# Performance work log

Measured on AMD Instinct MI355X. Metric: run time of the kernel, lower is better.

## Reference

```python
import jax, jax.numpy as jnp
import numpy as np
import math

N_HEAD, HEAD_DIM = 12, 64
TAU = 1.0


def setup_inputs() -> dict:
    key = jax.random.key(0)
    ks = jax.random.split(key, 4)
    B, T, C = 2, 2048, 768
    x = jax.random.normal(ks[0], (B, T, C), jnp.float32)
    # Linear params (stored as [in, out]; math-equivalent to torch's x @ W.T + b).
    # 0.02 init scale keeps attention logits in a realistic range.
    w_attn = jax.random.normal(ks[1], (C, 3 * N_HEAD * HEAD_DIM), jnp.float32) * 0.02
    b_attn = jnp.zeros((3 * N_HEAD * HEAD_DIM,), jnp.float32)
    w_proj = jax.random.normal(ks[2], (N_HEAD * HEAD_DIM, C), jnp.float32) * 0.02
    b_proj = jnp.zeros((C,), jnp.float32)
    return {"x": x, "w_attn": w_attn, "b_attn": b_attn, "w_proj": w_proj, "b_proj": b_proj}


def reference(x, w_attn, b_attn, w_proj, b_proj):
    B, T, C = x.shape
    nh, hd, tau = N_HEAD, HEAD_DIM, TAU

    qkv = x @ w_attn + b_attn                              # [B,T,3*nh*hd]
    q, k, v = jnp.split(qkv, 3, axis=2)
    to_heads = lambda t: t.reshape(B, T, nh, hd).transpose(0, 2, 1, 3)  # [B,nh,T,hd]
    q, k, v = to_heads(q), to_heads(k), to_heads(v)

    att = jnp.einsum('bhqd,bhkd->bhqk', q, k) * (1.0 / math.sqrt(hd))   # [B,nh,T,T]
    causal = jnp.tril(jnp.ones((T, T), bool))
    att = jnp.where(causal, att, -jnp.inf)

    # Memory-penalty built from head 0 scores.
    S = jax.nn.relu(att[:, 0])                             # [B,T,T]; relu(-inf)=0
    col = jnp.arange(T)
    keep = (col[None, :] != 0) & (col[:, None] != col[None, :])  # zero col 0 and diagonal
    S = S * keep
    # roll rows down by 1 with row 0 zeroed
    S_shifted = jnp.concatenate([jnp.zeros((B, 1, T), S.dtype), S[:, :-1]], axis=1)
    FF = jnp.cumsum(S_shifted, axis=-2)[:, None]           # [B,1,T,T]
    FF_sum = jnp.clip(FF, 0.0, tau).sum(axis=-1)           # [B,1,T]
    positions = jnp.arange(T, dtype=x.dtype).reshape(1, 1, T, 1)
    M = positions - FF_sum / tau                           # broadcasts to [1,B,T,T] (as torch does)

    att = jax.nn.softmax(att - FF, axis=-1)
    y = jnp.einsum('bhqk,bhkd->bhqd', att, v)              # [B,nh,T,hd]
    y = y.transpose(0, 2, 1, 3).reshape(B, T, nh * hd)
    y = y @ w_proj + b_proj
    return (y, M)
```

## Files before the change

kernel.cpp:

```cpp
#include <hip/hip_runtime.h>
#include <cstddef>

#define TT 2048
#define BB 2
#define CC 768
#define NH 12
#define HD 64
#define N3 2304
#define Y_ELEMS (BB*TT*CC)
#define M_ELEMS (BB*TT*TT)

typedef __attribute__((ext_vector_type(8))) short bf16x8;
typedef __attribute__((ext_vector_type(4))) float f32x4;

__device__ inline unsigned short f2b(float f) {
  union { float f; unsigned u; } v; v.f = f;
  unsigned r = (v.u + 0x7FFFu + ((v.u >> 16) & 1u)) >> 16;
  return (unsigned short)r;
}
__device__ inline float b2f(unsigned short u) {
  union { unsigned u; float f; } v; v.u = (unsigned)u << 16; return v.f;
}

__device__ inline void gload_lds16(const unsigned short* g, unsigned short* l) {
  __builtin_amdgcn_global_load_lds(
      (const __attribute__((address_space(1))) unsigned int*)g,
      (__attribute__((address_space(3))) unsigned int*)l, 16, 0, 0);
}

__global__ __launch_bounds__(256) void pack_x(
    const float* __restrict__ x, unsigned short* __restrict__ xb) {
  size_t i = ((size_t)blockIdx.x * 256 + threadIdx.x) * 8;
  float4 a = *(const float4*)(x + i);
  float4 b = *(const float4*)(x + i + 4);
  ushort4 o0, o1;
  o0.x = f2b(a.x); o0.y = f2b(a.y); o0.z = f2b(a.z); o0.w = f2b(a.w);
  o1.x = f2b(b.x); o1.y = f2b(b.y); o1.z = f2b(b.z); o1.w = f2b(b.w);
  *(ushort4*)(xb + i) = o0;
  *(ushort4*)(xb + i + 4) = o1;
}

__global__ __launch_bounds__(256) void transpose_pack(
    const float* __restrict__ W, unsigned short* __restrict__ WT, int N) {
  __shared__ float tile[64][65];
  int kt = blockIdx.x, nt = blockIdx.y;
  int tid = threadIdx.x;
  int r = tid >> 4, c4 = (tid & 15) << 2;
#pragma unroll
  for (int rep = 0; rep < 4; ++rep) {
    int row = rep * 16 + r;
    float4 v = *(const float4*)(W + (size_t)(kt * 64 + row) * N + nt * 64 + c4);
    tile[row][c4 + 0] = v.x; tile[row][c4 + 1] = v.y;
    tile[row][c4 + 2] = v.z; tile[row][c4 + 3] = v.w;
  }
  __syncthreads();
#pragma unroll
  for (int rep = 0; rep < 4; ++rep) {
    int nrow = rep * 16 + r;
    ushort4 o;
    o.x = f2b(tile[c4 + 0][nrow]); o.y = f2b(tile[c4 + 1][nrow]);
    o.z = f2b(tile[c4 + 2][nrow]); o.w = f2b(tile[c4 + 3][nrow]);
    *(ushort4*)(WT + (size_t)(nt * 64 + nrow) * CC + kt * 64 + c4) = o;
  }
}

__global__ __launch_bounds__(256, 3) void gemm_qkv_bf16(
    const unsigned short* __restrict__ xb, const unsigned short* __restrict__ wbT,
    const float* __restrict__ b_attn,
    unsigned short* __restrict__ Qb, unsigned short* __restrict__ Kb,
    unsigned short* __restrict__ Vt) {
  __shared__ __align__(16) unsigned short smem_u[17408];
  unsigned short (*Alds)[128][32] = (unsigned short(*)[128][32])smem_u;
  unsigned short (*Blds)[128][32] = (unsigned short(*)[128][32])(smem_u + 8192);
  unsigned short (*Vlds)[136]     = (unsigned short(*)[136])smem_u;

  int mt = blockIdx.x, nt = blockIdx.y;
  int sec = nt / 6, h0 = (nt % 6) * 2;
  int wave = threadIdx.x >> 6, lane = threadIdx.x & 63;
  int lr = lane & 15, lg = lane >> 4;
  int m0 = mt * 128;
  int n0 = nt * 128;

  int srow = lane >> 2;
  int sslot = (lane & 3) ^ (srow & 3);

#define STAGE_AB(BUF, K0)                                                       \
  {                                                                             \
    _Pragma("unroll")                                                           \
    for (int p = 0; p < 2; ++p) {                                               \
      int ar = wave * 32 + p * 16 + srow;                                       \
      gload_lds16(xb + (size_t)(m0 + ar) * CC + (K0) + (sslot << 3),            \
                  &Alds[BUF][wave * 32 + p * 16][0]);                           \
      gload_lds16(wbT + (size_t)(n0 + ar) * CC + (K0) + (sslot << 3),           \
                  &Blds[BUF][wave * 32 + p * 16][0]);                           \
    }                                                                           \
  }

  f32x4 acc[2][8];
#pragma unroll
  for (int mi = 0; mi < 2; ++mi)
#pragma unroll
    for (int nj = 0; nj < 8; ++nj) acc[mi][nj] = (f32x4){0.f, 0.f, 0.f, 0.f};

  STAGE_AB(0, 0)
  __syncthreads();

  int fslot = lg ^ (lr & 3);
  for (int kt = 0; kt < 24; ++kt) {
    int cur = kt & 1;
    if (kt < 23) STAGE_AB(cur ^ 1, (kt + 1) * 32)
    bf16x8 af[2], bf[8];
#pragma unroll
    for (int mi = 0; mi < 2; ++mi)
      af[mi] = *(const bf16x8*)&Alds[cur][wave * 32 + mi * 16 + lr][fslot << 3];
#pragma unroll
    for (int nj = 0; nj < 8; ++nj)
      bf[nj] = *(const bf16x8*)&Blds[cur][nj * 16 + lr][fslot << 3];
    __builtin_amdgcn_s_setprio(1);
#pragma unroll
    for (int nj = 0; nj < 8; ++nj)
#pragma unroll
      for (int mi = 0; mi < 2; ++mi)
        acc[mi][nj] = __builtin_amdgcn_mfma_f32_16x16x32_bf16(af[mi], bf[nj], acc[mi][nj], 0, 0, 0);
    __builtin_amdgcn_s_setprio(0);
    __syncthreads();
  }
#undef STAGE_AB

  int b = m0 >> 11;
  float bias[8];
#pragma unroll
  for (int nj = 0; nj < 8; ++nj) bias[nj] = b_attn[n0 + nj * 16 + lr];

  if (sec < 2) {
    float qscale = (sec == 0) ? 0.125f : 1.0f;
    unsigned short* OutB = (sec == 0 ? Qb : Kb);
    int tbase = (m0 & 2047) + wave * 32 + lg * 4;
#pragma unroll
    for (int nj = 0; nj < 8; ++nj) {
      int h = h0 + (nj >> 2);
      int d = (nj & 3) * 16 + lr;
      unsigned short* Out = OutB + (size_t)(b * NH + h) * TT * HD;
#pragma unroll
      for (int mi = 0; mi < 2; ++mi)
#pragma unroll
        for (int r = 0; r < 4; ++r) {
          int t = tbase + mi * 16 + r;
          Out[(size_t)t * HD + d] = f2b((acc[mi][nj][r] + bias[nj]) * qscale);
        }
    }
  } else {
    int tl = wave * 32 + lg * 4;
#pragma unroll
    for (int mi = 0; mi < 2; ++mi)
#pragma unroll
      for (int r = 0; r < 4; ++r)
#pragma unroll
        for (int nj = 0; nj < 8; ++nj)
          Vlds[tl + mi * 16 + r][nj * 16 + lr] = f2b(acc[mi][nj][r] + bias[nj]);
    __syncthreads();
    int d = threadIdx.x & 63, tc = threadIdx.x >> 6;
    int tblk = (m0 & 2047);
#pragma unroll
    for (int hh = 0; hh < 2; ++hh) {
      unsigned short* Ov = Vt + ((size_t)(b * NH + h0 + hh) * HD + d) * TT + tblk + tc * 32;
      int c = hh * 64 + d;
#pragma unroll
      for (int i8 = 0; i8 < 4; ++i8) {
        ushort4 o0, o1;
        o0.x = Vlds[tc * 32 + i8 * 8 + 0][c]; o0.y = Vlds[tc * 32 + i8 * 8 + 1][c];
        o0.z = Vlds[tc * 32 + i8 * 8 + 2][c]; o0.w = Vlds[tc * 32 + i8 * 8 + 3][c];
        o1.x = Vlds[tc * 32 + i8 * 8 + 4][c]; o1.y = Vlds[tc * 32 + i8 * 8 + 5][c];
        o1.z = Vlds[tc * 32 + i8 * 8 + 6][c]; o1.w = Vlds[tc * 32 + i8 * 8 + 7][c];
        *(ushort4*)(Ov + i8 * 8) = o0;
        *(ushort4*)(Ov + i8 * 8 + 4) = o1;
      }
    }
  }
}

__global__ __launch_bounds__(256, 3) void gemm_proj_bf16(
    const unsigned short* __restrict__ yhb, const unsigned short* __restrict__ wpT,
    const float* __restrict__ b_proj, float* __restrict__ y) {
  __shared__ __align__(16) unsigned short Alds[2][128][32];
  __shared__ __align__(16) unsigned short Blds[2][64][32];
  int mt = blockIdx.x, nt = blockIdx.y;
  int wave = threadIdx.x >> 6, lane = threadIdx.x & 63;
  int lr = lane & 15, lg = lane >> 4;
  int m0 = mt * 128;
  int n0 = nt * 64;

  int srow = lane >> 2;
  int sslot = (lane & 3) ^ (srow & 3);

#define STAGE_AB(BUF, K0)                                                       \
  {                                                                             \
    _Pragma("unroll")                                                           \
    for (int p = 0; p < 2; ++p) {                                               \
      int ar = wave * 32 + p * 16 + srow;                                       \
      gload_lds16(yhb + (size_t)(m0 + ar) * CC + (K0) + (sslot << 3),           \
                  &Alds[BUF][wave * 32 + p * 16][0]);                           \
    }                                                                           \
    int br = wave * 16 + srow;                                                  \
    gload_lds16(wpT + (size_t)(n0 + br) * CC + (K0) + (sslot << 3),             \
                &Blds[BUF][wave * 16][0]);                                      \
  }

  f32x4 acc[2][4];
#pragma unroll
  for (int mi = 0; mi < 2; ++mi)
#pragma unroll
    for (int nj = 0; nj < 4; ++nj) acc[mi][nj] = (f32x4){0.f, 0.f, 0.f, 0.f};

  STAGE_AB(0, 0)
  __syncthreads();

  int fslot = lg ^ (lr & 3);
  for (int kt = 0; kt < 24; ++kt) {
    int cur = kt & 1;
    if (kt < 23) STAGE_AB(cur ^ 1, (kt + 1) * 32)
    bf16x8 af[2], bf[4];
#pragma unroll
    for (int mi = 0; mi < 2; ++mi)
      af[mi] = *(const bf16x8*)&Alds[cur][wave * 32 + mi * 16 + lr][fslot << 3];
#pragma unroll
    for (int nj = 0; nj < 4; ++nj)
      bf[nj] = *(const bf16x8*)&Blds[cur][nj * 16 + lr][fslot << 3];
    __builtin_amdgcn_s_setprio(1);
#pragma unroll
    for (int nj = 0; nj < 4; ++nj)
#pragma unroll
      for (int mi = 0; mi < 2; ++mi)
        acc[mi][nj] = __builtin_amdgcn_mfma_f32_16x16x32_bf16(af[mi], bf[nj], acc[mi][nj], 0, 0, 0);
    __builtin_amdgcn_s_setprio(0);
    __syncthreads();
  }
#undef STAGE_AB

  float bias[4];
#pragma unroll
  for (int nj = 0; nj < 4; ++nj) bias[nj] = b_proj[n0 + nj * 16 + lr];
#pragma unroll
  for (int mi = 0; mi < 2; ++mi)
#pragma unroll
    for (int r = 0; r < 4; ++r) {
      int m = m0 + wave * 32 + mi * 16 + lg * 4 + r;
#pragma unroll
      for (int nj = 0; nj < 4; ++nj)
        y[(size_t)m * CC + n0 + nj * 16 + lr] = acc[mi][nj][r] + bias[nj];
    }
}

__global__ __launch_bounds__(256) void sgemm_qk0(
    const float* __restrict__ x, const float* __restrict__ w_attn,
    const float* __restrict__ b_attn, float* __restrict__ q0,
    float* __restrict__ k0) {
  __shared__ float As[16][32];
  __shared__ float Bs[16][64];
  int sec = blockIdx.y;
  const float* Bw = w_attn + sec * CC;
  float* Out = sec ? k0 : q0;
  int tid = threadIdx.x;
  int tx = tid & 15, ty = tid >> 4;
  int m0 = blockIdx.x * 32;

  int arow = tid >> 3;
  int acol2 = (tid & 7) << 1;
  int brow = tid >> 4;
  int bcol4 = (tid & 15) << 2;

  const float* Aptr = x + (size_t)(m0 + arow) * CC + acol2;
  const float* Bptr = Bw + (size_t)brow * N3 + bcol4;

  float acc[2][4] = {};

  for (int k0_ = 0; k0_ < CC; k0_ += 16) {
    float2 av = *(const float2*)(Aptr + k0_);
    float4 bv = *(const float4*)(Bptr + (size_t)k0_ * N3);
    As[acol2 + 0][arow] = av.x;
    As[acol2 + 1][arow] = av.y;
    *(float4*)&Bs[brow][bcol4] = bv;
    __syncthreads();
#pragma unroll
    for (int kk = 0; kk < 16; ++kk) {
      float2 a2 = *(const float2*)&As[kk][ty << 1];
      float4 b4 = *(const float4*)&Bs[kk][tx << 2];
      float a[2] = {a2.x, a2.y};
      float b[4] = {b4.x, b4.y, b4.z, b4.w};
#pragma unroll
      for (int ii = 0; ii < 2; ++ii)
#pragma unroll
        for (int jj = 0; jj < 4; ++jj) acc[ii][jj] += a[ii] * b[jj];
    }
    __syncthreads();
  }

  float4 bv = *(const float4*)(b_attn + sec * CC + (tx << 2));
#pragma unroll
  for (int ii = 0; ii < 2; ++ii) {
    int m = m0 + (ty << 1) + ii;
    float4 o;
    o.x = acc[ii][0] + bv.x;
    o.y = acc[ii][1] + bv.y;
    o.z = acc[ii][2] + bv.z;
    o.w = acc[ii][3] + bv.w;
    *(float4*)(Out + (size_t)m * HD + (tx << 2)) = o;
  }
}

__global__ __launch_bounds__(256) void score0_kernel(
    const float* __restrict__ q0, const float* __restrict__ k0,
    float* __restrict__ Sbuf, float* __restrict__ partials) {
  int it = blockIdx.x, jt = blockIdx.y, b = blockIdx.z;
  int tid = threadIdx.x;
  int i0 = it * 64, j0 = jt * 64;
  if (jt > it) {
    if (tid < 64) partials[((size_t)(b * 32 + it)) * TT + j0 + tid] = 0.f;
    return;
  }
  __shared__ float Qs[64][64];
  __shared__ float Ks[64][64];
  int row = tid >> 2;
  int dq = (tid & 3) << 2;
  const float* qb = q0 + (size_t)((b * TT) + i0 + row) * HD;
  const float* kb = k0 + (size_t)((b * TT) + j0 + row) * HD;
#pragma unroll
  for (int rep = 0; rep < 4; ++rep) {
    int d = dq + rep * 16;
    float4 qv = *(const float4*)(qb + d);
    float4 kv = *(const float4*)(kb + d);
    Qs[d + 0][row] = qv.x; Qs[d + 1][row] = qv.y;
    Qs[d + 2][row] = qv.z; Qs[d + 3][row] = qv.w;
    Ks[d + 0][row] = kv.x; Ks[d + 1][row] = kv.y;
    Ks[d + 2][row] = kv.z; Ks[d + 3][row] = kv.w;
  }
  __syncthreads();
  int tx = tid & 15, ty = tid >> 4;
  float acc[4][4] = {};
#pragma unroll 8
  for (int kk = 0; kk < 64; ++kk) {
    float4 a4 = *(const float4*)&Qs[kk][ty << 2];
    float4 b4 = *(const float4*)&Ks[kk][tx << 2];
    float a[4] = {a4.x, a4.y, a4.z, a4.w};
    float b[4] = {b4.x, b4.y, b4.z, b4.w};
#pragma unroll
    for (int ii = 0; ii < 4; ++ii)
#pragma unroll
      for (int jj = 0; jj < 4; ++jj) acc[ii][jj] += a[ii] * b[jj];
  }
  float red4[4] = {0.f, 0.f, 0.f, 0.f};
#pragma unroll
  for (int ii = 0; ii < 4; ++ii) {
    int r = i0 + (ty << 2) + ii;
    int gi = (b * TT) + r;
    float ov[4];
#pragma unroll
    for (int jj = 0; jj < 4; ++jj) {
      ov[jj] = fmaxf(acc[ii][jj] * 0.125f, 0.f);
      int j = j0 + (tx << 2) + jj;
      if (j >= 1 && j < r) red4[jj] += ov[jj];
    }
    float4 o; o.x = ov[0]; o.y = ov[1]; o.z = ov[2]; o.w = ov[3];
    *(float4*)(Sbuf + (size_t)gi * TT + j0 + (tx << 2)) = o;
  }
  __syncthreads();
  *(float4*)&Qs[ty][tx << 2] = *(float4*)red4;
  __syncthreads();
  if (tid < 64) {
    float cs = 0.f;
#pragma unroll
    for (int t = 0; t < 16; ++t) cs += Qs[t][tid];
    partials[((size_t)(b * 32 + it)) * TT + j0 + tid] = cs;
  }
}

__global__ __launch_bounds__(256) void scan_write(
    const float* __restrict__ Sbuf, const float* __restrict__ partials,
    unsigned short* __restrict__ Eb, float* __restrict__ ffpart) {
  int j = blockIdx.x * 256 + threadIdx.x;
  int chunk = blockIdx.y, b = blockIdx.z;
  float run = 0.f;
  for (int c = 0; c < chunk; ++c) run += partials[((size_t)(b * 32 + c)) * TT + j];
  int r0 = chunk * 64;
  int jswz = (j & ~63) | ((j & 15) << 2) | ((j >> 4) & 3);
  const float* base = Sbuf + (size_t)(b * TT + r0) * TT + j;
  unsigned short* ebase = Eb + (size_t)(b * TT + r0) * TT + jswz;
  __shared__ float wsum[4][64];
  int wv = threadIdx.x >> 6;
  for (int rb = 0; rb < 64; rb += 8) {
    float v[8];
#pragma unroll
    for (int u = 0; u < 8; ++u) {
      int r = r0 + rb + u;
      v[u] = (j >= 1 && j < r) ? base[(size_t)(rb + u) * TT] : 0.f;
    }
#pragma unroll
    for (int u = 0; u < 8; ++u) {
      int rr = rb + u;
      ebase[(size_t)rr * TT] = f2b(__expf(-run));
      float c1 = fminf(run, 1.f);
#pragma unroll
      for (int o = 1; o < 64; o <<= 1) c1 += __shfl_xor(c1, o);
      if ((threadIdx.x & 63) == 0) wsum[wv][rr] = c1;
      run += v[u];
    }
  }
  __syncthreads();
  if (threadIdx.x < 64)
    ffpart[((size_t)(b * 8) + blockIdx.x) * TT + r0 + threadIdx.x] =
        wsum[0][threadIdx.x] + wsum[1][threadIdx.x] +
        wsum[2][threadIdx.x] + wsum[3][threadIdx.x];
}

__global__ __launch_bounds__(256, 3) void attn_mfma(
    const unsigned short* __restrict__ Qb, const unsigned short* __restrict__ Kb,
    const unsigned short* __restrict__ Vt, const unsigned short* __restrict__ Eb,
    unsigned short* __restrict__ yhb) {
  int xbh = blockIdx.x;
  int b = (xbh >> 2) & 1;
  int h = ((xbh >> 3) << 2) | (xbh & 3);
  int g4 = 31 - (int)blockIdx.y;
  int wave = threadIdx.x >> 6, lane = threadIdx.x & 63;
  int lr = lane & 15, lg = lane >> 4;
  int i0 = g4 * 64 + wave * 16;
  int bh = b * NH + h;
  const unsigned short* Qh = Qb + (size_t)bh * TT * HD;
  const unsigned short* Kh = Kb + (size_t)bh * TT * HD;
  const unsigned short* Vh = Vt + (size_t)bh * HD * TT;
  const unsigned short* Erow = Eb + ((size_t)(b * TT) + i0 + lg * 4) * TT + 4 * lr;

  __shared__ __align__(16) unsigned short Ksh[2][64][64];
  __shared__ __align__(16) unsigned short Vsh[2][64][64];
  __shared__ __align__(16) unsigned short Plds[4][16][80];

  int rowoff = lane >> 3;
  int sslot  = (lane & 7) ^ rowoff;

  bf16x8 qf[2];
#pragma unroll
  for (int ks = 0; ks < 2; ++ks)
    qf[ks] = *(const bf16x8*)(Qh + (size_t)(i0 + lr) * HD + ks * 32 + lg * 8);

  f32x4 acc[4];
  float lrun[4] = {0.f, 0.f, 0.f, 0.f};
#pragma unroll
  for (int q = 0; q < 4; ++q) acc[q] = (f32x4){0.f, 0.f, 0.f, 0.f};

#define STAGE_KV(BUF, J0)                                                      \
  {                                                                            \
    _Pragma("unroll")                                                          \
    for (int p = 0; p < 2; ++p) {                                              \
      int r0 = wave * 16 + p * 8;                                              \
      gload_lds16(Kh + (size_t)((J0) + r0 + rowoff) * HD + sslot * 8,          \
                  &Ksh[BUF][r0][0]);                                           \
      gload_lds16(Vh + (size_t)(r0 + rowoff) * TT + (J0) + sslot * 8,          \
                  &Vsh[BUF][r0][0]);                                           \
    }                                                                          \
  }

  STAGE_KV(0, 0)
  __syncthreads();

  for (int kt = 0; kt <= g4; ++kt) {
    int cur = kt & 1;
    int j0 = kt * 64;
    if (kt < g4) STAGE_KV(cur ^ 1, j0 + 64)

    ushort4 ev[4];
#pragma unroll
    for (int r = 0; r < 4; ++r)
      ev[r] = *(const ushort4*)(Erow + (size_t)r * TT + j0);

    f32x4 s[4];
    __builtin_amdgcn_s_setprio(1);
#pragma unroll
    for (int nj = 0; nj < 4; ++nj) {
      int row = nj * 16 + lr;
      int sw = row & 7;
      bf16x8 k0f = *(const bf16x8*)&Ksh[cur][row][(lg ^ sw) << 3];
      bf16x8 k1f = *(const bf16x8*)&Ksh[cur][row][((4 + lg) ^ sw) << 3];
      f32x4 z = (f32x4){0.f, 0.f, 0.f, 0.f};
      z = __builtin_amdgcn_mfma_f32_16x16x32_bf16(qf[0], k0f, z, 0, 0, 0);
      s[nj] = __builtin_amdgcn_mfma_f32_16x16x32_bf16(qf[1], k1f, z, 0, 0, 0);
    }
    __builtin_amdgcn_s_setprio(0);

    int ibase = i0 + lg * 4;
    if (kt == g4) {
#pragma unroll
      for (int nj = 0; nj < 4; ++nj)
#pragma unroll
        for (int r = 0; r < 4; ++r)
          if (j0 + nj * 16 + lr > ibase + r) s[nj][r] = -1e30f;
    }

#pragma unroll
    for (int r = 0; r < 4; ++r) {
      float p0 = b2f(ev[r].x) * __expf(s[0][r]);
      float p1 = b2f(ev[r].y) * __expf(s[1][r]);
      float p2 = b2f(ev[r].z) * __expf(s[2][r]);
      float p3 = b2f(ev[r].w) * __expf(s[3][r]);
      lrun[r] += (p0 + p1) + (p2 + p3);
      Plds[wave][lg * 4 + r][0 * 16 + lr] = f2b(p0);
      Plds[wave][lg * 4 + r][1 * 16 + lr] = f2b(p1);
      Plds[wave][lg * 4 + r][2 * 16 + lr] = f2b(p2);
      Plds[wave][lg * 4 + r][3 * 16 + lr] = f2b(p3);
    }

    bf16x8 pa0 = *(const bf16x8*)&Plds[wave][lr][lg * 8];
    bf16x8 pa1 = *(const bf16x8*)&Plds[wave][lr][32 + lg * 8];
    __builtin_amdgcn_s_setprio(1);
#pragma unroll
    for (int nd = 0; nd < 4; ++nd) {
      int row = nd * 16 + lr;
      int sw = row & 7;
      bf16x8 v0f = *(const bf16x8*)&Vsh[cur][row][(lg ^ sw) << 3];
      bf16x8 v1f = *(const bf16x8*)&Vsh[cur][row][((4 + lg) ^ sw) << 3];
      acc[nd] = __builtin_amdgcn_mfma_f32_16x16x32_bf16(pa0, v0f, acc[nd], 0, 0, 0);
      acc[nd] = __builtin_amdgcn_mfma_f32_16x16x32_bf16(pa1, v1f, acc[nd], 0, 0, 0);
    }
    __builtin_amdgcn_s_setprio(0);

    __syncthreads();
  }
#undef STAGE_KV

#pragma unroll
  for (int r = 0; r < 4; ++r) {
    lrun[r] += __shfl_xor(lrun[r], 1);
    lrun[r] += __shfl_xor(lrun[r], 2);
    lrun[r] += __shfl_xor(lrun[r], 4);
    lrun[r] += __shfl_xor(lrun[r], 8);
    float inv = 1.f / lrun[r];
    int ig = i0 + lg * 4 + r;
    unsigned short* ob = yhb + (size_t)(b * TT + ig) * CC + h * HD;
#pragma unroll
    for (int nd = 0; nd < 4; ++nd)
      ob[nd * 16 + lr] = f2b(acc[nd][r] * inv);
  }
}

__global__ __launch_bounds__(256) void m_kernel(
    const float* __restrict__ ffpart, float* __restrict__ Mout) {
  int idx4 = blockIdx.x * blockDim.x + threadIdx.x;
  int stride = gridDim.x * blockDim.x;
  for (; idx4 < M_ELEMS / 4; idx4 += stride) {
    int idx = idx4 << 2;
    int j = idx & (TT - 1);
    int i = (idx >> 11) & (TT - 1);
    int b = idx >> 22;
    const float* fp = ffpart + ((size_t)(b * 8)) * TT + j;
    float4 s = make_float4(0.f, 0.f, 0.f, 0.f);
#pragma unroll
    for (int p = 0; p < 8; ++p) {
      float4 v = *(const float4*)(fp + (size_t)p * TT);
      s.x += v.x; s.y += v.y; s.z += v.z; s.w += v.w;
    }
    float fi = (float)i;
    float4 o = make_float4(fi - s.x, fi - s.y, fi - s.z, fi - s.w);
    *(float4*)(Mout + idx) = o;
  }
}

extern "C" void kernel_launch(void* const* d_in, const int* in_sizes, int n_in,
                              void* d_out, int out_size, void* d_ws, size_t ws_size,
                              hipStream_t stream) {
  const float* x      = (const float*)d_in[0];
  const float* w_attn = (const float*)d_in[1];
  const float* b_attn = (const float*)d_in[2];
  const float* w_proj = (const float*)d_in[3];
  const float* b_proj = (const float*)d_in[4];

  float* y    = (float*)d_out;
  float* Mreg = y + Y_ELEMS;

  float* ws = (float*)d_ws;
  float* q0       = ws;
  float* k0       = q0 + (size_t)BB * TT * HD;
  float* partials = k0 + (size_t)BB * TT * HD;
  float* ffpart   = partials + (size_t)BB * 32 * TT;
  unsigned short* xb  = (unsigned short*)(ffpart + (size_t)BB * 8 * TT);
  unsigned short* wbT = xb + (size_t)Y_ELEMS;
  unsigned short* wpT = wbT + (size_t)N3 * CC;
  unsigned short* Qb  = wpT + (size_t)CC * CC;
  unsigned short* Kb  = Qb + (size_t)BB * NH * TT * HD;
  unsigned short* Vt  = Kb + (size_t)BB * NH * TT * HD;
  unsigned short* yhb = Vt + (size_t)BB * NH * TT * HD;
  unsigned short* Eb  = yhb + (size_t)Y_ELEMS;

  pack_x<<<Y_ELEMS / (256 * 8), 256, 0, stream>>>(x, xb);
  transpose_pack<<<dim3(CC / 64, N3 / 64), 256, 0, stream>>>(w_attn, wbT, N3);
  transpose_pack<<<dim3(CC / 64, CC / 64), 256, 0, stream>>>(w_proj, wpT, CC);
  gemm_qkv_bf16<<<dim3(32, 18), 256, 0, stream>>>(xb, wbT, b_attn, Qb, Kb, Vt);
  sgemm_qk0<<<dim3(128, 2), 256, 0, stream>>>(x, w_attn, b_attn, q0, k0);
  score0_kernel<<<dim3(32, 32, BB), 256, 0, stream>>>(q0, k0, Mreg, partials);
  scan_write<<<dim3(8, 32, BB), 256, 0, stream>>>(Mreg, partials, Eb, ffpart);
  attn_mfma<<<dim3(24, 32), 256, 0, stream>>>(Qb, Kb, Vt, Eb, yhb);
  m_kernel<<<4096, 256, 0, stream>>>(ffpart, Mreg);
  gemm_proj_bf16<<<dim3(32, 12), 256, 0, stream>>>(yhb, wpT, b_proj, y);
}
```

Before: 192.3 us.

## Merge prep, qk0 sgemm, proj and M kernels into fewer launches

Merges pack_x and both weight transposes into one prep kernel, and folds the fp32 head-0 q/k sgemm into the QKV GEMM grid as extra block rows, retiled to 128-row blocks. The M-output fill and the projection GEMM now share one grid with a block-index split. The attention kernel's query-tile order is interleaved so long and short causal tiles alternate. The aim is to cut launch overhead and let independent work share the GPU at once; the cost is larger, branchier kernels whose shared launch bounds and LDS sizing may limit occupancy for some roles.

```diff
diff --git a/kernel.cpp b/kernel.cpp
--- a/kernel.cpp
+++ b/kernel.cpp
@@ -28,23 +28,37 @@
       (__attribute__((address_space(3))) unsigned int*)l, 16, 0, 0);
 }
 
-__global__ __launch_bounds__(256) void pack_x(
-    const float* __restrict__ x, unsigned short* __restrict__ xb) {
-  size_t i = ((size_t)blockIdx.x * 256 + threadIdx.x) * 8;
-  float4 a = *(const float4*)(x + i);
-  float4 b = *(const float4*)(x + i + 4);
-  ushort4 o0, o1;
-  o0.x = f2b(a.x); o0.y = f2b(a.y); o0.z = f2b(a.z); o0.w = f2b(a.w);
-  o1.x = f2b(b.x); o1.y = f2b(b.y); o1.z = f2b(b.z); o1.w = f2b(b.w);
-  *(ushort4*)(xb + i) = o0;
-  *(ushort4*)(xb + i + 4) = o1;
-}
-
-__global__ __launch_bounds__(256) void transpose_pack(
-    const float* __restrict__ W, unsigned short* __restrict__ WT, int N) {
+__global__ __launch_bounds__(256) void prep_fused(
+    const float* __restrict__ x, const float* __restrict__ w_attn,
+    const float* __restrict__ w_proj,
+    unsigned short* __restrict__ xb, unsigned short* __restrict__ wbT,
+    unsigned short* __restrict__ wpT) {
+  int bid = blockIdx.x;
+  int tid = threadIdx.x;
+  if (bid < 1536) {
+    size_t i = ((size_t)bid * 256 + tid) * 8;
+    float4 a = *(const float4*)(x + i);
+    float4 b = *(const float4*)(x + i + 4);
+    ushort4 o0, o1;
+    o0.x = f2b(a.x); o0.y = f2b(a.y); o0.z = f2b(a.z); o0.w = f2b(a.w);
+    o1.x = f2b(b.x); o1.y = f2b(b.y); o1.z = f2b(b.z); o1.w = f2b(b.w);
+    *(ushort4*)(xb + i) = o0;
+    *(ushort4*)(xb + i + 4) = o1;
+    return;
+  }
+  const float* W;
+  unsigned short* WT;
+  int N, kt, nt;
+  if (bid < 1968) {
+    int t = bid - 1536;
+    W = w_attn; WT = wbT; N = N3;
+    kt = t % 12; nt = t / 12;
+  } else {
+    int t = bid - 1968;
+    W = w_proj; WT = wpT; N = CC;
+    kt = t % 12; nt = t / 12;
+  }
   __shared__ float tile[64][65];
-  int kt = blockIdx.x, nt = blockIdx.y;
-  int tid = threadIdx.x;
   int r = tid >> 4, c4 = (tid & 15) << 2;
 #pragma unroll
   for (int rep = 0; rep < 4; ++rep) {
@@ -64,17 +78,75 @@
   }
 }
 
-__global__ __launch_bounds__(256, 3) void gemm_qkv_bf16(
+__global__ __launch_bounds__(256, 3) void gemm_qkv_fused(
     const unsigned short* __restrict__ xb, const unsigned short* __restrict__ wbT,
     const float* __restrict__ b_attn,
     unsigned short* __restrict__ Qb, unsigned short* __restrict__ Kb,
-    unsigned short* __restrict__ Vt) {
+    unsigned short* __restrict__ Vt,
+    const float* __restrict__ x, const float* __restrict__ w_attn,
+    float* __restrict__ q0, float* __restrict__ k0) {
   __shared__ __align__(16) unsigned short smem_u[17408];
+  int mt = blockIdx.x, nt = blockIdx.y;
+
+  if (nt >= 18) {
+    int sec = nt - 18;
+    const float* Bw = w_attn + sec * CC;
+    float* Out = sec ? k0 : q0;
+    float (*As)[132] = (float(*)[132])smem_u;
+    float (*Bs)[68]  = (float(*)[68])(smem_u + 4224 * 2);
+    int tid = threadIdx.x;
+    int tx = tid & 15, ty = tid >> 4;
+    int m0 = mt * 128;
+    int arow = tid >> 2, acol4 = (tid & 3) << 2;
+    int brow = tid >> 4, bcol4 = (tid & 15) << 2;
+
+    const float* Aptr = x + (size_t)(m0 + arow) * CC + acol4;
+    const float* Bptr = Bw + (size_t)brow * N3 + bcol4;
+
+    float acc[8][4] = {};
+    for (int k0_ = 0; k0_ < CC; k0_ += 16) {
+#pragma unroll
+      for (int rep = 0; rep < 2; ++rep) {
+        float4 av = *(const float4*)(Aptr + (size_t)rep * 64 * CC + k0_);
+        As[acol4 + 0][arow + rep * 64] = av.x;
+        As[acol4 + 1][arow + rep * 64] = av.y;
+        As[acol4 + 2][arow + rep * 64] = av.z;
+        As[acol4 + 3][arow + rep * 64] = av.w;
+      }
+      float4 bv = *(const float4*)(Bptr + (size_t)k0_ * N3);
+      *(float4*)&Bs[brow][bcol4] = bv;
+      __syncthreads();
+#pragma unroll
+      for (int kk = 0; kk < 16; ++kk) {
+        float b4[4];
+        *(float4*)b4 = *(const float4*)&Bs[kk][tx << 2];
+#pragma unroll
+        for (int ii = 0; ii < 8; ++ii) {
+          float a = As[kk][ty * 8 + ii];
+#pragma unroll
+          for (int jj = 0; jj < 4; ++jj) acc[ii][jj] += a * b4[jj];
+        }
+      }
+      __syncthreads();
+    }
+    float4 bv = *(const float4*)(b_attn + sec * CC + (tx << 2));
+#pragma unroll
+    for (int ii = 0; ii < 8; ++ii) {
+      int m = m0 + ty * 8 + ii;
+      float4 o;
+      o.x = acc[ii][0] + bv.x;
+      o.y = acc[ii][1] + bv.y;
+      o.z = acc[ii][2] + bv.z;
+      o.w = acc[ii][3] + bv.w;
+      *(float4*)(Out + (size_t)m * HD + (tx << 2)) = o;
+    }
+    return;
+  }
+
   unsigned short (*Alds)[128][32] = (unsigned short(*)[128][32])smem_u;
   unsigned short (*Blds)[128][32] = (unsigned short(*)[128][32])(smem_u + 8192);
   unsigned short (*Vlds)[136]     = (unsigned short(*)[136])smem_u;
 
-  int mt = blockIdx.x, nt = blockIdx.y;
   int sec = nt / 6, h0 = (nt % 6) * 2;
   int wave = threadIdx.x >> 6, lane = threadIdx.x & 63;
   int lr = lane & 15, lg = lane >> 4;
@@ -176,135 +248,6 @@
         *(ushort4*)(Ov + i8 * 8 + 4) = o1;
       }
     }
-  }
-}
-
-__global__ __launch_bounds__(256, 3) void gemm_proj_bf16(
-    const unsigned short* __restrict__ yhb, const unsigned short* __restrict__ wpT,
-    const float* __restrict__ b_proj, float* __restrict__ y) {
-  __shared__ __align__(16) unsigned short Alds[2][128][32];
-  __shared__ __align__(16) unsigned short Blds[2][64][32];
-  int mt = blockIdx.x, nt = blockIdx.y;
-  int wave = threadIdx.x >> 6, lane = threadIdx.x & 63;
-  int lr = lane & 15, lg = lane >> 4;
-  int m0 = mt * 128;
-  int n0 = nt * 64;
-
-  int srow = lane >> 2;
-  int sslot = (lane & 3) ^ (srow & 3);
-
-#define STAGE_AB(BUF, K0)                                                       \
-  {                                                                             \
-    _Pragma("unroll")                                                           \
-    for (int p = 0; p < 2; ++p) {                                               \
-      int ar = wave * 32 + p * 16 + srow;                                       \
-      gload_lds16(yhb + (size_t)(m0 + ar) * CC + (K0) + (sslot << 3),           \
-                  &Alds[BUF][wave * 32 + p * 16][0]);                           \
-    }                                                                           \
-    int br = wave * 16 + srow;                                                  \
-    gload_lds16(wpT + (size_t)(n0 + br) * CC + (K0) + (sslot << 3),             \
-                &Blds[BUF][wave * 16][0]);                                      \
-  }
-
-  f32x4 acc[2][4];
-#pragma unroll
-  for (int mi = 0; mi < 2; ++mi)
-#pragma unroll
-    for (int nj = 0; nj < 4; ++nj) acc[mi][nj] = (f32x4){0.f, 0.f, 0.f, 0.f};
-
-  STAGE_AB(0, 0)
-  __syncthreads();
-
-  int fslot = lg ^ (lr & 3);
-  for (int kt = 0; kt < 24; ++kt) {
-    int cur = kt & 1;
-    if (kt < 23) STAGE_AB(cur ^ 1, (kt + 1) * 32)
-    bf16x8 af[2], bf[4];
-#pragma unroll
-    for (int mi = 0; mi < 2; ++mi)
-      af[mi] = *(const bf16x8*)&Alds[cur][wave * 32 + mi * 16 + lr][fslot << 3];
-#pragma unroll
-    for (int nj = 0; nj < 4; ++nj)
-      bf[nj] = *(const bf16x8*)&Blds[cur][nj * 16 + lr][fslot << 3];
-    __builtin_amdgcn_s_setprio(1);
-#pragma unroll
-    for (int nj = 0; nj < 4; ++nj)
-#pragma unroll
-      for (int mi = 0; mi < 2; ++mi)
-        acc[mi][nj] = __builtin_amdgcn_mfma_f32_16x16x32_bf16(af[mi], bf[nj], acc[mi][nj], 0, 0, 0);
-    __builtin_amdgcn_s_setprio(0);
-    __syncthreads();
-  }
-#undef STAGE_AB
-
-  float bias[4];
-#pragma unroll
-  for (int nj = 0; nj < 4; ++nj) bias[nj] = b_proj[n0 + nj * 16 + lr];
-#pragma unroll
-  for (int mi = 0; mi < 2; ++mi)
-#pragma unroll
-    for (int r = 0; r < 4; ++r) {
-      int m = m0 + wave * 32 + mi * 16 + lg * 4 + r;
-#pragma unroll
-      for (int nj = 0; nj < 4; ++nj)
-        y[(size_t)m * CC + n0 + nj * 16 + lr] = acc[mi][nj][r] + bias[nj];
-    }
-}
-
-__global__ __launch_bounds__(256) void sgemm_qk0(
-    const float* __restrict__ x, const float* __restrict__ w_attn,
-    const float* __restrict__ b_attn, float* __restrict__ q0,
-    float* __restrict__ k0) {
-  __shared__ float As[16][32];
-  __shared__ float Bs[16][64];
-  int sec = blockIdx.y;
-  const float* Bw = w_attn + sec * CC;
-  float* Out = sec ? k0 : q0;
-  int tid = threadIdx.x;
-  int tx = tid & 15, ty = tid >> 4;
-  int m0 = blockIdx.x * 32;
-
-  int arow = tid >> 3;
-  int acol2 = (tid & 7) << 1;
-  int brow = tid >> 4;
-  int bcol4 = (tid & 15) << 2;
-
-  const float* Aptr = x + (size_t)(m0 + arow) * CC + acol2;
-  const float* Bptr = Bw + (size_t)brow * N3 + bcol4;
-
-  float acc[2][4] = {};
-
-  for (int k0_ = 0; k0_ < CC; k0_ += 16) {
-    float2 av = *(const float2*)(Aptr + k0_);
-    float4 bv = *(const float4*)(Bptr + (size_t)k0_ * N3);
-    As[acol2 + 0][arow] = av.x;
-    As[acol2 + 1][arow] = av.y;
-    *(float4*)&Bs[brow][bcol4] = bv;
-    __syncthreads();
-#pragma unroll
-    for (int kk = 0; kk < 16; ++kk) {
-      float2 a2 = *(const float2*)&As[kk][ty << 1];
-      float4 b4 = *(const float4*)&Bs[kk][tx << 2];
-      float a[2] = {a2.x, a2.y};
-      float b[4] = {b4.x, b4.y, b4.z, b4.w};
-#pragma unroll
-      for (int ii = 0; ii < 2; ++ii)
-#pragma unroll
-        for (int jj = 0; jj < 4; ++jj) acc[ii][jj] += a[ii] * b[jj];
-    }
-    __syncthreads();
-  }
-
-  float4 bv = *(const float4*)(b_attn + sec * CC + (tx << 2));
-#pragma unroll
-  for (int ii = 0; ii < 2; ++ii) {
-    int m = m0 + (ty << 1) + ii;
-    float4 o;
-    o.x = acc[ii][0] + bv.x;
-    o.y = acc[ii][1] + bv.y;
-    o.z = acc[ii][2] + bv.z;
-    o.w = acc[ii][3] + bv.w;
-    *(float4*)(Out + (size_t)m * HD + (tx << 2)) = o;
   }
 }
 
@@ -419,7 +362,8 @@
   int xbh = blockIdx.x;
   int b = (xbh >> 2) & 1;
   int h = ((xbh >> 3) << 2) | (xbh & 3);
-  int g4 = 31 - (int)blockIdx.y;
+  int yy = blockIdx.y;
+  int g4 = (yy & 1) ? (yy >> 1) : (31 - (yy >> 1));
   int wave = threadIdx.x >> 6, lane = threadIdx.x & 63;
   int lr = lane & 15, lg = lane >> 4;
   int i0 = g4 * 64 + wave * 16;
@@ -540,26 +484,99 @@
   }
 }
 
-__global__ __launch_bounds__(256) void m_kernel(
+__global__ __launch_bounds__(256, 3) void proj_m_fused(
+    const unsigned short* __restrict__ yhb, const unsigned short* __restrict__ wpT,
+    const float* __restrict__ b_proj, float* __restrict__ y,
     const float* __restrict__ ffpart, float* __restrict__ Mout) {
-  int idx4 = blockIdx.x * blockDim.x + threadIdx.x;
-  int stride = gridDim.x * blockDim.x;
-  for (; idx4 < M_ELEMS / 4; idx4 += stride) {
-    int idx = idx4 << 2;
-    int j = idx & (TT - 1);
-    int i = (idx >> 11) & (TT - 1);
-    int b = idx >> 22;
-    const float* fp = ffpart + ((size_t)(b * 8)) * TT + j;
-    float4 s = make_float4(0.f, 0.f, 0.f, 0.f);
-#pragma unroll
-    for (int p = 0; p < 8; ++p) {
-      float4 v = *(const float4*)(fp + (size_t)p * TT);
-      s.x += v.x; s.y += v.y; s.z += v.z; s.w += v.w;
-    }
-    float fi = (float)i;
-    float4 o = make_float4(fi - s.x, fi - s.y, fi - s.z, fi - s.w);
-    *(float4*)(Mout + idx) = o;
-  }
+  int bid = blockIdx.x;
+  if (bid >= 384) {
+    int idx4 = (bid - 384) * 256 + threadIdx.x;
+    int stride = (gridDim.x - 384) * 256;
+    for (; idx4 < M_ELEMS / 4; idx4 += stride) {
+      int idx = idx4 << 2;
+      int j = idx & (TT - 1);
+      int i = (idx >> 11) & (TT - 1);
+      int b = idx >> 22;
+      const float* fp = ffpart + ((size_t)(b * 8)) * TT + j;
+      float4 s = make_float4(0.f, 0.f, 0.f, 0.f);
+#pragma unroll
+      for (int p = 0; p < 8; ++p) {
+        float4 v = *(const float4*)(fp + (size_t)p * TT);
+        s.x += v.x; s.y += v.y; s.z += v.z; s.w += v.w;
+      }
+      float fi = (float)i;
+      float4 o = make_float4(fi - s.x, fi - s.y, fi - s.z, fi - s.w);
+      *(float4*)(Mout + idx) = o;
+    }
+    return;
+  }
+  __shared__ __align__(16) unsigned short Alds[2][128][32];
+  __shared__ __align__(16) unsigned short Blds[2][64][32];
+  int mt = bid & 31, nt = bid >> 5;
+  int wave = threadIdx.x >> 6, lane = threadIdx.x & 63;
+  int lr = lane & 15, lg = lane >> 4;
+  int m0 = mt * 128;
+  int n0 = nt * 64;
+
+  int srow = lane >> 2;
+  int sslot = (lane & 3) ^ (srow & 3);
+
+#define STAGE_AB(BUF, K0)                                                       \
+  {                                                                             \
+    _Pragma("unroll")                                                           \
+    for (int p = 0; p < 2; ++p) {                                               \
+      int ar = wave * 32 + p * 16 + srow;                                       \
+      gload_lds16(yhb + (size_t)(m0 + ar) * CC + (K0) + (sslot << 3),           \
+                  &Alds[BUF][wave * 32 + p * 16][0]);                           \
+    }                                                                           \
+    int br = wave * 16 + srow;                                                  \
+    gload_lds16(wpT + (size_t)(n0 + br) * CC + (K0) + (sslot << 3),             \
+                &Blds[BUF][wave * 16][0]);                                      \
+  }
+
+  f32x4 acc[2][4];
+#pragma unroll
+  for (int mi = 0; mi < 2; ++mi)
+#pragma unroll
+    for (int nj = 0; nj < 4; ++nj) acc[mi][nj] = (f32x4){0.f, 0.f, 0.f, 0.f};
+
+  STAGE_AB(0, 0)
+  __syncthreads();
+
+  int fslot = lg ^ (lr & 3);
+  for (int kt = 0; kt < 24; ++kt) {
+    int cur = kt & 1;
+    if (kt < 23) STAGE_AB(cur ^ 1, (kt + 1) * 32)
+    bf16x8 af[2], bf[4];
+#pragma unroll
+    for (int mi = 0; mi < 2; ++mi)
+      af[mi] = *(const bf16x8*)&Alds[cur][wave * 32 + mi * 16 + lr][fslot << 3];
+#pragma unroll
+    for (int nj = 0; nj < 4; ++nj)
+      bf[nj] = *(const bf16x8*)&Blds[cur][nj * 16 + lr][fslot << 3];
+    __builtin_amdgcn_s_setprio(1);
+#pragma unroll
+    for (int nj = 0; nj < 4; ++nj)
+#pragma unroll
+      for (int mi = 0; mi < 2; ++mi)
+        acc[mi][nj] = __builtin_amdgcn_mfma_f32_16x16x32_bf16(af[mi], bf[nj], acc[mi][nj], 0, 0, 0);
+    __builtin_amdgcn_s_setprio(0);
+    __syncthreads();
+  }
+#undef STAGE_AB
+
+  float bias[4];
+#pragma unroll
+  for (int nj = 0; nj < 4; ++nj) bias[nj] = b_proj[n0 + nj * 16 + lr];
+#pragma unroll
+  for (int mi = 0; mi < 2; ++mi)
+#pragma unroll
+    for (int r = 0; r < 4; ++r) {
+      int m = m0 + wave * 32 + mi * 16 + lg * 4 + r;
+#pragma unroll
+      for (int nj = 0; nj < 4; ++nj)
+        y[(size_t)m * CC + n0 + nj * 16 + lr] = acc[mi][nj][r] + bias[nj];
+    }
 }
 
 extern "C" void kernel_launch(void* const* d_in, const int* in_sizes, int n_in,
@@ -588,14 +605,11 @@
   unsigned short* yhb = Vt + (size_t)BB * NH * TT * HD;
   unsigned short* Eb  = yhb + (size_t)Y_ELEMS;
 
-  pack_x<<<Y_ELEMS / (256 * 8), 256, 0, stream>>>(x, xb);
-  transpose_pack<<<dim3(CC / 64, N3 / 64), 256, 0, stream>>>(w_attn, wbT, N3);
-  transpose_pack<<<dim3(CC / 64, CC / 64), 256, 0, stream>>>(w_proj, wpT, CC);
-  gemm_qkv_bf16<<<dim3(32, 18), 256, 0, stream>>>(xb, wbT, b_attn, Qb, Kb, Vt);
-  sgemm_qk0<<<dim3(128, 2), 256, 0, stream>>>(x, w_attn, b_attn, q0, k0);
+  prep_fused<<<2112, 256, 0, stream>>>(x, w_attn, w_proj, xb, wbT, wpT);
+  gemm_qkv_fused<<<dim3(32, 20), 256, 0, stream>>>(
+      xb, wbT, b_attn, Qb, Kb, Vt, x, w_attn, q0, k0);
   score0_kernel<<<dim3(32, 32, BB), 256, 0, stream>>>(q0, k0, Mreg, partials);
   scan_write<<<dim3(8, 32, BB), 256, 0, stream>>>(Mreg, partials, Eb, ffpart);
   attn_mfma<<<dim3(24, 32), 256, 0, stream>>>(Qb, Kb, Vt, Eb, yhb);
-  m_kernel<<<4096, 256, 0, stream>>>(ffpart, Mreg);
-  gemm_proj_bf16<<<dim3(32, 12), 256, 0, stream>>>(yhb, wpT, b_proj, y);
-}
+  proj_m_fused<<<1408, 256, 0, stream>>>(yhb, wpT, b_proj, y, ffpart, Mreg);
+}
```

Measured after the change: 191.4 us. Within noise of the previous version (-0.4%).

## Fuse prep kernels and proj GEMM with M writer; interleave attention row order

Applied to the files above, without the earlier changes.

Merges pack_x and the two transpose_pack launches into one prep kernel, and merges the M-output writer with the projection GEMM into a single launch with role-split blocks. Attention blocks now alternate heavy and light causal row tiles so the work per wave of blocks is more even. This removes launch gaps and lets the memory-bound M write overlap the compute-bound projection GEMM. The cost is heavier per-block branching, and the fused kernel's launch bounds and shared memory now apply to the M blocks too.

```diff
diff --git a/kernel.cpp b/kernel.cpp
--- a/kernel.cpp
+++ b/kernel.cpp
@@ -28,23 +28,37 @@
       (__attribute__((address_space(3))) unsigned int*)l, 16, 0, 0);
 }
 
-__global__ __launch_bounds__(256) void pack_x(
-    const float* __restrict__ x, unsigned short* __restrict__ xb) {
-  size_t i = ((size_t)blockIdx.x * 256 + threadIdx.x) * 8;
-  float4 a = *(const float4*)(x + i);
-  float4 b = *(const float4*)(x + i + 4);
-  ushort4 o0, o1;
-  o0.x = f2b(a.x); o0.y = f2b(a.y); o0.z = f2b(a.z); o0.w = f2b(a.w);
-  o1.x = f2b(b.x); o1.y = f2b(b.y); o1.z = f2b(b.z); o1.w = f2b(b.w);
-  *(ushort4*)(xb + i) = o0;
-  *(ushort4*)(xb + i + 4) = o1;
-}
-
-__global__ __launch_bounds__(256) void transpose_pack(
-    const float* __restrict__ W, unsigned short* __restrict__ WT, int N) {
+__global__ __launch_bounds__(256) void prep_fused(
+    const float* __restrict__ x, const float* __restrict__ w_attn,
+    const float* __restrict__ w_proj,
+    unsigned short* __restrict__ xb, unsigned short* __restrict__ wbT,
+    unsigned short* __restrict__ wpT) {
+  int bid = blockIdx.x;
+  int tid = threadIdx.x;
+  if (bid < 1536) {
+    size_t i = ((size_t)bid * 256 + tid) * 8;
+    float4 a = *(const float4*)(x + i);
+    float4 b = *(const float4*)(x + i + 4);
+    ushort4 o0, o1;
+    o0.x = f2b(a.x); o0.y = f2b(a.y); o0.z = f2b(a.z); o0.w = f2b(a.w);
+    o1.x = f2b(b.x); o1.y = f2b(b.y); o1.z = f2b(b.z); o1.w = f2b(b.w);
+    *(ushort4*)(xb + i) = o0;
+    *(ushort4*)(xb + i + 4) = o1;
+    return;
+  }
+  const float* W;
+  unsigned short* WT;
+  int N, kt, nt;
+  if (bid < 1968) {
+    int t = bid - 1536;
+    W = w_attn; WT = wbT; N = N3;
+    kt = t % 12; nt = t / 12;
+  } else {
+    int t = bid - 1968;
+    W = w_proj; WT = wpT; N = CC;
+    kt = t % 12; nt = t / 12;
+  }
   __shared__ float tile[64][65];
-  int kt = blockIdx.x, nt = blockIdx.y;
-  int tid = threadIdx.x;
   int r = tid >> 4, c4 = (tid & 15) << 2;
 #pragma unroll
   for (int rep = 0; rep < 4; ++rep) {
@@ -177,78 +191,6 @@
       }
     }
   }
-}
-
-__global__ __launch_bounds__(256, 3) void gemm_proj_bf16(
-    const unsigned short* __restrict__ yhb, const unsigned short* __restrict__ wpT,
-    const float* __restrict__ b_proj, float* __restrict__ y) {
-  __shared__ __align__(16) unsigned short Alds[2][128][32];
-  __shared__ __align__(16) unsigned short Blds[2][64][32];
-  int mt = blockIdx.x, nt = blockIdx.y;
-  int wave = threadIdx.x >> 6, lane = threadIdx.x & 63;
-  int lr = lane & 15, lg = lane >> 4;
-  int m0 = mt * 128;
-  int n0 = nt * 64;
-
-  int srow = lane >> 2;
-  int sslot = (lane & 3) ^ (srow & 3);
-
-#define STAGE_AB(BUF, K0)                                                       \
-  {                                                                             \
-    _Pragma("unroll")                                                           \
-    for (int p = 0; p < 2; ++p) {                                               \
-      int ar = wave * 32 + p * 16 + srow;                                       \
-      gload_lds16(yhb + (size_t)(m0 + ar) * CC + (K0) + (sslot << 3),           \
-                  &Alds[BUF][wave * 32 + p * 16][0]);                           \
-    }                                                                           \
-    int br = wave * 16 + srow;                                                  \
-    gload_lds16(wpT + (size_t)(n0 + br) * CC + (K0) + (sslot << 3),             \
-                &Blds[BUF][wave * 16][0]);                                      \
-  }
-
-  f32x4 acc[2][4];
-#pragma unroll
-  for (int mi = 0; mi < 2; ++mi)
-#pragma unroll
-    for (int nj = 0; nj < 4; ++nj) acc[mi][nj] = (f32x4){0.f, 0.f, 0.f, 0.f};
-
-  STAGE_AB(0, 0)
-  __syncthreads();
-
-  int fslot = lg ^ (lr & 3);
-  for (int kt = 0; kt < 24; ++kt) {
-    int cur = kt & 1;
-    if (kt < 23) STAGE_AB(cur ^ 1, (kt + 1) * 32)
-    bf16x8 af[2], bf[4];
-#pragma unroll
-    for (int mi = 0; mi < 2; ++mi)
-      af[mi] = *(const bf16x8*)&Alds[cur][wave * 32 + mi * 16 + lr][fslot << 3];
-#pragma unroll
-    for (int nj = 0; nj < 4; ++nj)
-      bf[nj] = *(const bf16x8*)&Blds[cur][nj * 16 + lr][fslot << 3];
-    __builtin_amdgcn_s_setprio(1);
-#pragma unroll
-    for (int nj = 0; nj < 4; ++nj)
-#pragma unroll
-      for (int mi = 0; mi < 2; ++mi)
-        acc[mi][nj] = __builtin_amdgcn_mfma_f32_16x16x32_bf16(af[mi], bf[nj], acc[mi][nj], 0, 0, 0);
-    __builtin_amdgcn_s_setprio(0);
-    __syncthreads();
-  }
-#undef STAGE_AB
-
-  float bias[4];
-#pragma unroll
-  for (int nj = 0; nj < 4; ++nj) bias[nj] = b_proj[n0 + nj * 16 + lr];
-#pragma unroll
-  for (int mi = 0; mi < 2; ++mi)
-#pragma unroll
-    for (int r = 0; r < 4; ++r) {
-      int m = m0 + wave * 32 + mi * 16 + lg * 4 + r;
-#pragma unroll
-      for (int nj = 0; nj < 4; ++nj)
-        y[(size_t)m * CC + n0 + nj * 16 + lr] = acc[mi][nj][r] + bias[nj];
-    }
 }
 
 __global__ __launch_bounds__(256) void sgemm_qk0(
@@ -419,7 +361,8 @@
   int xbh = blockIdx.x;
   int b = (xbh >> 2) & 1;
   int h = ((xbh >> 3) << 2) | (xbh & 3);
-  int g4 = 31 - (int)blockIdx.y;
+  int yy = blockIdx.y;
+  int g4 = (yy & 1) ? (yy >> 1) : (31 - (yy >> 1));
   int wave = threadIdx.x >> 6, lane = threadIdx.x & 63;
   int lr = lane & 15, lg = lane >> 4;
   int i0 = g4 * 64 + wave * 16;
@@ -540,26 +483,99 @@
   }
 }
 
-__global__ __launch_bounds__(256) void m_kernel(
+__global__ __launch_bounds__(256, 3) void proj_m_fused(
+    const unsigned short* __restrict__ yhb, const unsigned short* __restrict__ wpT,
+    const float* __restrict__ b_proj, float* __restrict__ y,
     const float* __restrict__ ffpart, float* __restrict__ Mout) {
-  int idx4 = blockIdx.x * blockDim.x + threadIdx.x;
-  int stride = gridDim.x * blockDim.x;
-  for (; idx4 < M_ELEMS / 4; idx4 += stride) {
-    int idx = idx4 << 2;
-    int j = idx & (TT - 1);
-    int i = (idx >> 11) & (TT - 1);
-    int b = idx >> 22;
-    const float* fp = ffpart + ((size_t)(b * 8)) * TT + j;
-    float4 s = make_float4(0.f, 0.f, 0.f, 0.f);
-#pragma unroll
-    for (int p = 0; p < 8; ++p) {
-      float4 v = *(const float4*)(fp + (size_t)p * TT);
-      s.x += v.x; s.y += v.y; s.z += v.z; s.w += v.w;
-    }
-    float fi = (float)i;
-    float4 o = make_float4(fi - s.x, fi - s.y, fi - s.z, fi - s.w);
-    *(float4*)(Mout + idx) = o;
-  }
+  int bid = blockIdx.x;
+  if (bid >= 384) {
+    int idx4 = (bid - 384) * 256 + threadIdx.x;
+    int stride = (gridDim.x - 384) * 256;
+    for (; idx4 < M_ELEMS / 4; idx4 += stride) {
+      int idx = idx4 << 2;
+      int j = idx & (TT - 1);
+      int i = (idx >> 11) & (TT - 1);
+      int b = idx >> 22;
+      const float* fp = ffpart + ((size_t)(b * 8)) * TT + j;
+      float4 s = make_float4(0.f, 0.f, 0.f, 0.f);
+#pragma unroll
+      for (int p = 0; p < 8; ++p) {
+        float4 v = *(const float4*)(fp + (size_t)p * TT);
+        s.x += v.x; s.y += v.y; s.z += v.z; s.w += v.w;
+      }
+      float fi = (float)i;
+      float4 o = make_float4(fi - s.x, fi - s.y, fi - s.z, fi - s.w);
+      *(float4*)(Mout + idx) = o;
+    }
+    return;
+  }
+  __shared__ __align__(16) unsigned short Alds[2][128][32];
+  __shared__ __align__(16) unsigned short Blds[2][64][32];
+  int mt = bid & 31, nt = bid >> 5;
+  int wave = threadIdx.x >> 6, lane = threadIdx.x & 63;
+  int lr = lane & 15, lg = lane >> 4;
+  int m0 = mt * 128;
+  int n0 = nt * 64;
+
+  int srow = lane >> 2;
+  int sslot = (lane & 3) ^ (srow & 3);
+
+#define STAGE_AB(BUF, K0)                                                       \
+  {                                                                             \
+    _Pragma("unroll")                                                           \
+    for (int p = 0; p < 2; ++p) {                                               \
+      int ar = wave * 32 + p * 16 + srow;                                       \
+      gload_lds16(yhb + (size_t)(m0 + ar) * CC + (K0) + (sslot << 3),           \
+                  &Alds[BUF][wave * 32 + p * 16][0]);                           \
+    }                                                                           \
+    int br = wave * 16 + srow;                                                  \
+    gload_lds16(wpT + (size_t)(n0 + br) * CC + (K0) + (sslot << 3),             \
+                &Blds[BUF][wave * 16][0]);                                      \
+  }
+
+  f32x4 acc[2][4];
+#pragma unroll
+  for (int mi = 0; mi < 2; ++mi)
+#pragma unroll
+    for (int nj = 0; nj < 4; ++nj) acc[mi][nj] = (f32x4){0.f, 0.f, 0.f, 0.f};
+
+  STAGE_AB(0, 0)
+  __syncthreads();
+
+  int fslot = lg ^ (lr & 3);
+  for (int kt = 0; kt < 24; ++kt) {
+    int cur = kt & 1;
+    if (kt < 23) STAGE_AB(cur ^ 1, (kt + 1) * 32)
+    bf16x8 af[2], bf[4];
+#pragma unroll
+    for (int mi = 0; mi < 2; ++mi)
+      af[mi] = *(const bf16x8*)&Alds[cur][wave * 32 + mi * 16 + lr][fslot << 3];
+#pragma unroll
+    for (int nj = 0; nj < 4; ++nj)
+      bf[nj] = *(const bf16x8*)&Blds[cur][nj * 16 + lr][fslot << 3];
+    __builtin_amdgcn_s_setprio(1);
+#pragma unroll
+    for (int nj = 0; nj < 4; ++nj)
+#pragma unroll
+      for (int mi = 0; mi < 2; ++mi)
+        acc[mi][nj] = __builtin_amdgcn_mfma_f32_16x16x32_bf16(af[mi], bf[nj], acc[mi][nj], 0, 0, 0);
+    __builtin_amdgcn_s_setprio(0);
+    __syncthreads();
+  }
+#undef STAGE_AB
+
+  float bias[4];
+#pragma unroll
+  for (int nj = 0; nj < 4; ++nj) bias[nj] = b_proj[n0 + nj * 16 + lr];
+#pragma unroll
+  for (int mi = 0; mi < 2; ++mi)
+#pragma unroll
+    for (int r = 0; r < 4; ++r) {
+      int m = m0 + wave * 32 + mi * 16 + lg * 4 + r;
+#pragma unroll
+      for (int nj = 0; nj < 4; ++nj)
+        y[(size_t)m * CC + n0 + nj * 16 + lr] = acc[mi][nj][r] + bias[nj];
+    }
 }
 
 extern "C" void kernel_launch(void* const* d_in, const int* in_sizes, int n_in,
@@ -588,14 +604,11 @@
   unsigned short* yhb = Vt + (size_t)BB * NH * TT * HD;
   unsigned short* Eb  = yhb + (size_t)Y_ELEMS;
 
-  pack_x<<<Y_ELEMS / (256 * 8), 256, 0, stream>>>(x, xb);
-  transpose_pack<<<dim3(CC / 64, N3 / 64), 256, 0, stream>>>(w_attn, wbT, N3);
-  transpose_pack<<<dim3(CC / 64, CC / 64), 256, 0, stream>>>(w_proj, wpT, CC);
+  prep_fused<<<2112, 256, 0, stream>>>(x, w_attn, w_proj, xb, wbT, wpT);
   gemm_qkv_bf16<<<dim3(32, 18), 256, 0, stream>>>(xb, wbT, b_attn, Qb, Kb, Vt);
   sgemm_qk0<<<dim3(128, 2), 256, 0, stream>>>(x, w_attn, b_attn, q0, k0);
   score0_kernel<<<dim3(32, 32, BB), 256, 0, stream>>>(q0, k0, Mreg, partials);
   scan_write<<<dim3(8, 32, BB), 256, 0, stream>>>(Mreg, partials, Eb, ffpart);
   attn_mfma<<<dim3(24, 32), 256, 0, stream>>>(Qb, Kb, Vt, Eb, yhb);
-  m_kernel<<<4096, 256, 0, stream>>>(ffpart, Mreg);
-  gemm_proj_bf16<<<dim3(32, 12), 256, 0, stream>>>(yhb, wpT, b_proj, y);
-}
+  proj_m_fused<<<1408, 256, 0, stream>>>(yhb, wpT, b_proj, y, ffpart, Mreg);
+}
```

Measured after the change: 177.3 us. 7.8% less time.
